# Kernel optimization log

Hardware: AMD Instinct MI355X
Metric: run time of the kernel (lower is better)

The kernel has to match this reference:

```python
import jax, jax.numpy as jnp
import numpy as np

DIM = 2048
NUM_HEADS = 16
HEAD_DIM = DIM // NUM_HEADS  # 128
LC = HEAD_DIM // 2           # 64 complex pairs per head
B, S = 2, 2048
EPS = 1e-6


def setup_inputs() -> dict:
    key = jax.random.key(0)
    ks = jax.random.split(key, 12)
    x = jax.random.normal(ks[0], (B, S, DIM), dtype=jnp.float32)
    # freqs: unit-modulus complex rotations stored as (cos, sin), shape [S,1,LC,2]
    theta = jax.random.uniform(ks[1], (S, 1, LC), dtype=jnp.float32) * (2.0 * np.pi)
    freqs = jnp.stack([jnp.cos(theta), jnp.sin(theta)], axis=-1)
    scale = 0.02
    wq = jax.random.normal(ks[2], (DIM, DIM), dtype=jnp.float32) * scale
    bq = jnp.zeros((DIM,), dtype=jnp.float32)
    wk = jax.random.normal(ks[3], (DIM, DIM), dtype=jnp.float32) * scale
    bk = jnp.zeros((DIM,), dtype=jnp.float32)
    wv = jax.random.normal(ks[4], (DIM, DIM), dtype=jnp.float32) * scale
    bv = jnp.zeros((DIM,), dtype=jnp.float32)
    wo = jax.random.normal(ks[5], (DIM, DIM), dtype=jnp.float32) * scale
    bo = jnp.zeros((DIM,), dtype=jnp.float32)
    gq = jnp.ones((DIM,), dtype=jnp.float32)   # RMSNorm weight for q
    gk = jnp.ones((DIM,), dtype=jnp.float32)   # RMSNorm weight for k
    return {"x": x, "freqs": freqs, "wq": wq, "bq": bq, "wk": wk, "bk": bk,
            "wv": wv, "bv": bv, "wo": wo, "bo": bo, "gq": gq, "gk": gk}


def _rms_norm(x, g):
    xf = x.astype(jnp.float32)
    y = xf * jax.lax.rsqrt(jnp.mean(xf * xf, axis=-1, keepdims=True) + EPS)
    return y.astype(x.dtype) * g


def _rope_apply(x, freqs):
    # x: [B,S,D] -> complex pairs [B,S,H,LC,2]; freqs: [S,1,LC,2] (cos,sin)
    b, s, _ = x.shape
    xp = x.astype(jnp.float32).reshape(b, s, NUM_HEADS, LC, 2)
    xr, xi = xp[..., 0], xp[..., 1]
    cr = freqs[None, :, :, :, 0]  # [1,S,1,LC]
    ci = freqs[None, :, :, :, 1]
    out_r = xr * cr - xi * ci
    out_i = xr * ci + xi * cr
    out = jnp.stack([out_r, out_i], axis=-1).reshape(b, s, DIM)
    return out.astype(x.dtype)


def _attention(q, k, v):
    # q,k,v: [B,S,D] -> multihead SDPA -> [B,S,D]
    b, s, _ = q.shape
    qh = q.reshape(b, s, NUM_HEADS, HEAD_DIM).transpose(0, 2, 1, 3)
    kh = k.reshape(b, s, NUM_HEADS, HEAD_DIM).transpose(0, 2, 1, 3)
    vh = v.reshape(b, s, NUM_HEADS, HEAD_DIM).transpose(0, 2, 1, 3)
    scale = 1.0 / np.sqrt(HEAD_DIM).astype(np.float32)
    scores = jnp.einsum('bhqd,bhkd->bhqk', qh, kh) * scale
    probs = jax.nn.softmax(scores, axis=-1)
    out = jnp.einsum('bhqk,bhkd->bhqd', probs, vh)
    return out.transpose(0, 2, 1, 3).reshape(b, s, DIM)


def reference(x, freqs, wq, bq, wk, bk, wv, bv, wo, bo, gq, gk):
    q = _rms_norm(x @ wq.T + bq, gq)
    k = _rms_norm(x @ wk.T + bk, gk)
    v = x @ wv.T + bv
    q = _rope_apply(q, freqs)
    k = _rope_apply(k, freqs)
    attn = _attention(q, k, v)
    return attn @ wo.T + bo
```

## Files before the change

kernel.cpp:

```cpp
#include <hip/hip_runtime.h>
#include <cstdint>

typedef __bf16 bf16;
typedef __bf16 bf16x8 __attribute__((ext_vector_type(8)));
typedef __bf16 bf16x4 __attribute__((ext_vector_type(4)));
typedef float f32x4 __attribute__((ext_vector_type(4)));

#define DIMN 2048
#define SEQ  2048
#define NH   16
#define HD   128

__device__ __forceinline__ void gld_lds16(const bf16* g, bf16* l) {
    __builtin_amdgcn_global_load_lds(
        (const __attribute__((address_space(1))) void*)g,
        (__attribute__((address_space(3))) void*)l,
        16, 0, 0);
}

__global__ __launch_bounds__(256) void cast_all(
    const float* __restrict__ x,
    const float* __restrict__ wq, const float* __restrict__ wk,
    const float* __restrict__ wv, const float* __restrict__ wo,
    bf16* __restrict__ xb,
    bf16* __restrict__ wqb, bf16* __restrict__ wkb,
    bf16* __restrict__ wvb, bf16* __restrict__ wob)
{
    int id = blockIdx.x;
    const float* src; bf16* dst; int i;
    if (id < 8192) { src = x; dst = xb; i = id * 256 + threadIdx.x; }
    else {
        id -= 8192;
        int w = id >> 12; id &= 4095;
        src = (w == 0) ? wq : (w == 1) ? wk : (w == 2) ? wv : wo;
        dst = (w == 0) ? wqb : (w == 1) ? wkb : (w == 2) ? wvb : wob;
        i = id * 256 + threadIdx.x;
    }
    float4 v = ((const float4*)src)[i];
    bf16x4 o;
    o[0] = (bf16)v.x; o[1] = (bf16)v.y; o[2] = (bf16)v.z; o[3] = (bf16)v.w;
    ((bf16x4*)dst)[i] = o;
}

template<int OUT_F32>
__global__ __launch_bounds__(256) void gemm_bt(
    const bf16* __restrict__ A,
    const bf16* __restrict__ Bw0, const bf16* __restrict__ Bw1, const bf16* __restrict__ Bw2,
    const float* __restrict__ bias0, const float* __restrict__ bias1, const float* __restrict__ bias2,
    void* __restrict__ C0, void* __restrict__ C1, void* __restrict__ C2)
{
    const int K = DIMN, N = DIMN;
    const bf16* Bw = Bw0; const float* bias = bias0; void* Cout = C0;
    if (blockIdx.z == 1) { Bw = Bw1; bias = bias1; Cout = C1; }
    if (blockIdx.z == 2) { Bw = Bw2; bias = bias2; Cout = C2; }

    __shared__ __attribute__((aligned(16))) bf16 As[128 * 64];
    __shared__ __attribute__((aligned(16))) bf16 Bs[128 * 64];

    const int t    = threadIdx.x;
    const int lane = t & 63, wave = t >> 6;
    const int l15  = lane & 15, quad = lane >> 4;
    const int wm   = (wave >> 1) * 64, wn = (wave & 1) * 64;
    const long bm  = (long)blockIdx.y * 128;
    const long bn  = (long)blockIdx.x * 128;

    const bf16* agp[4]; const bf16* bgp[4]; bf16* asd[4]; bf16* bsd[4];
#pragma unroll
    for (int it = 0; it < 4; it++) {
        int fs  = it * 256 + t;
        int row = fs >> 3;
        int gs  = (fs & 7) ^ (row & 7);
        agp[it] = A  + (bm + row) * (long)K + gs * 8;
        bgp[it] = Bw + (bn + row) * (long)K + gs * 8;
        asd[it] = As + fs * 8;
        bsd[it] = Bs + fs * 8;
    }
    const int swl = l15 & 7;

    f32x4 acc[4][4] = {};

    for (int k0 = 0; k0 < K; k0 += 64) {
#pragma unroll
        for (int it = 0; it < 4; it++) {
            gld_lds16(agp[it] + k0, asd[it]);
            gld_lds16(bgp[it] + k0, bsd[it]);
        }
        __syncthreads();

#pragma unroll
        for (int ks2 = 0; ks2 < 2; ks2++) {
            const int sw = ((ks2 * 4 + quad) ^ swl) * 8;
            bf16x8 af[4], bfr[4];
#pragma unroll
            for (int i = 0; i < 4; i++)
                af[i] = *(const bf16x8*)(As + (wm + i * 16 + l15) * 64 + sw);
#pragma unroll
            for (int j = 0; j < 4; j++)
                bfr[j] = *(const bf16x8*)(Bs + (wn + j * 16 + l15) * 64 + sw);
#pragma unroll
            for (int i = 0; i < 4; i++)
#pragma unroll
                for (int j = 0; j < 4; j++)
                    acc[i][j] = __builtin_amdgcn_mfma_f32_16x16x32_bf16(af[i], bfr[j], acc[i][j], 0, 0, 0);
        }
        __syncthreads();
    }

#pragma unroll
    for (int j = 0; j < 4; j++) {
        const long col = bn + wn + j * 16 + l15;
        const float bv = bias[col];
#pragma unroll
        for (int i = 0; i < 4; i++) {
            const long row0 = bm + wm + i * 16 + quad * 4;
#pragma unroll
            for (int r = 0; r < 4; r++) {
                float v = acc[i][j][r] + bv;
                if (OUT_F32) ((float*)Cout)[(row0 + r) * N + col] = v;
                else         ((bf16*)Cout)[(row0 + r) * N + col] = (bf16)v;
            }
        }
    }
}

__global__ __launch_bounds__(256) void norm_prep(
    bf16* __restrict__ q, bf16* __restrict__ k,
    const float* __restrict__ gq, const float* __restrict__ gk,
    const float* __restrict__ freqs,
    const bf16* __restrict__ vin, bf16* __restrict__ vt)
{
    const int id = blockIdx.x;
    const int t = threadIdx.x;
    if (id < 8192) {
        const int qk  = id >> 12;
        const int row = id & 4095;
        bf16* ptr = qk ? k : q;
        const float* g = qk ? gk : gq;
        const float osc = qk ? 1.0f : 0.08838834764831845f;
        const int s = row & (SEQ - 1);
        const int lane = t & 63, wave = t >> 6;

        bf16* base = ptr + (long)row * DIMN + t * 8;
        bf16x8 raw = *(const bf16x8*)base;
        float v[8]; float ss = 0.f;
#pragma unroll
        for (int j = 0; j < 8; j++) { v[j] = (float)raw[j]; ss += v[j] * v[j]; }
#pragma unroll
        for (int off = 32; off; off >>= 1) ss += __shfl_xor(ss, off, 64);
        __shared__ float red[4];
        if (lane == 0) red[wave] = ss;
        __syncthreads();
        float tot = red[0] + red[1] + red[2] + red[3];
        float rn = rsqrtf(tot * (1.0f / DIMN) + 1e-6f);

        const int e0 = t * 8;
        bf16x8 o;
#pragma unroll
        for (int pp = 0; pp < 4; pp++) {
            int e = e0 + pp * 2;
            float xr = v[pp * 2]     * rn * g[e];
            float xi = v[pp * 2 + 1] * rn * g[e + 1];
            int lc = (e >> 1) & 63;
            float cr = freqs[s * 128 + lc * 2];
            float ci = freqs[s * 128 + lc * 2 + 1];
            o[pp * 2]     = (bf16)((xr * cr - xi * ci) * osc);
            o[pp * 2 + 1] = (bf16)((xr * ci + xi * cr) * osc);
        }
        *(bf16x8*)base = o;
    } else {
        const int tid = id - 8192;
        const int b = tid >> 10, rem = tid & 1023;
        const int st = rem & 31, ct = rem >> 5;
        __shared__ float tile[64][65];
        const int tx = t & 63, ty = t >> 6;
#pragma unroll
        for (int ii = 0; ii < 16; ii++) {
            int r = ii * 4 + ty;
            tile[r][tx] = (float)vin[((long)(b * SEQ + st * 64 + r)) * DIMN + ct * 64 + tx];
        }
        __syncthreads();
#pragma unroll
        for (int ii = 0; ii < 16; ii++) {
            int c = ii * 4 + ty;
            vt[((long)(b * DIMN + ct * 64 + c)) * SEQ + st * 64 + tx] = (bf16)tile[tx][c];
        }
    }
}

__global__ __launch_bounds__(512, 2) void attention(
    const bf16* __restrict__ Q, const bf16* __restrict__ Kb,
    const bf16* __restrict__ Vt, bf16* __restrict__ O)
{
    __shared__ __attribute__((aligned(16))) bf16 Ksh[2][64 * 128];
    __shared__ __attribute__((aligned(16))) bf16 Vsh[2][128 * 64];
    __shared__ __attribute__((aligned(16))) bf16 Psh[8][32 * 72];
    __shared__ float Lsh[8][32];

    const int t = threadIdx.x;
    const int lane = t & 63, w = t >> 6;
    const int l15 = lane & 15, quad = lane >> 4;
    const int bh = blockIdx.x, b = bh >> 4, h = bh & 15;
    const int qt = blockIdx.y;
    const long qrow0 = (long)b * SEQ + qt * 256 + w * 32;
    const bf16* qbase = Q  + qrow0 * DIMN + h * HD;
    const bf16* kbase = Kb + (long)b * SEQ * DIMN + h * HD;
    const bf16* vbase = Vt + (long)bh * HD * SEQ;

    bf16x8 qf[2][4];
#pragma unroll
    for (int im = 0; im < 2; im++)
#pragma unroll
        for (int kd = 0; kd < 4; kd++)
            qf[im][kd] = *(const bf16x8*)(qbase + (long)(im * 16 + l15) * DIMN + kd * 32 + quad * 8);

    long koff[2], voff[2];
#pragma unroll
    for (int it = 0; it < 2; it++) {
        int fs = it * 512 + t;
        int kr = fs >> 4, kp = fs & 15;
        koff[it] = (long)kr * DIMN + (kp ^ (kr & 15)) * 8;
        int dr = fs >> 3, vp = fs & 7;
        voff[it] = (long)dr * SEQ + (vp ^ (dr & 7)) * 8;
    }

    f32x4 o_acc[2][8] = {};
    float Lt[2] = {0.f, 0.f};

#pragma unroll
    for (int it = 0; it < 2; it++) {
        gld_lds16(kbase + koff[it], &Ksh[0][(it * 512 + t) * 8]);
        gld_lds16(vbase + voff[it], &Vsh[0][(it * 512 + t) * 8]);
    }
    __syncthreads();

    for (int kt = 0; kt < 32; kt++) {
        const int cur = kt & 1;
        if (kt < 31) {
            const bf16* kg = kbase + (long)((kt + 1) * 64) * DIMN;
            const bf16* vg = vbase + (kt + 1) * 64;
#pragma unroll
            for (int it = 0; it < 2; it++) {
                gld_lds16(kg + koff[it], &Ksh[cur ^ 1][(it * 512 + t) * 8]);
                gld_lds16(vg + voff[it], &Vsh[cur ^ 1][(it * 512 + t) * 8]);
            }
        }
        const bf16* K0 = Ksh[cur];
        const bf16* V0 = Vsh[cur];

        f32x4 st[4][2] = {};
#pragma unroll
        for (int jk = 0; jk < 4; jk++)
#pragma unroll
            for (int kd = 0; kd < 4; kd++) {
                bf16x8 kf = *(const bf16x8*)(K0 + (jk * 16 + l15) * 128 + (((kd * 4 + quad) ^ l15) & 15) * 8);
                st[jk][0] = __builtin_amdgcn_mfma_f32_16x16x32_bf16(kf, qf[0][kd], st[jk][0], 0, 0, 0);
                st[jk][1] = __builtin_amdgcn_mfma_f32_16x16x32_bf16(kf, qf[1][kd], st[jk][1], 0, 0, 0);
            }

#pragma unroll
        for (int im = 0; im < 2; im++) {
            float part = 0.f;
#pragma unroll
            for (int jk = 0; jk < 4; jk++) {
                bf16x4 pk;
#pragma unroll
                for (int r = 0; r < 4; r++) {
                    float e = __expf(st[jk][im][r]);
                    part += e;
                    pk[r] = (bf16)e;
                }
                *(bf16x4*)(Psh[w] + (im * 16 + l15) * 72 + jk * 16 + quad * 4) = pk;
            }
            Lt[im] += part;
        }

#pragma unroll
        for (int kd2 = 0; kd2 < 2; kd2++) {
            bf16x8 pa[2];
            pa[0] = *(const bf16x8*)(Psh[w] + (l15)      * 72 + kd2 * 32 + quad * 8);
            pa[1] = *(const bf16x8*)(Psh[w] + (16 + l15) * 72 + kd2 * 32 + quad * 8);
#pragma unroll
            for (int dj = 0; dj < 8; dj++) {
                bf16x8 vfr = *(const bf16x8*)(V0 + (dj * 16 + l15) * 64 + (((kd2 * 4 + quad) ^ l15) & 7) * 8);
                o_acc[0][dj] = __builtin_amdgcn_mfma_f32_16x16x32_bf16(pa[0], vfr, o_acc[0][dj], 0, 0, 0);
                o_acc[1][dj] = __builtin_amdgcn_mfma_f32_16x16x32_bf16(pa[1], vfr, o_acc[1][dj], 0, 0, 0);
            }
        }
        __syncthreads();
    }

#pragma unroll
    for (int im = 0; im < 2; im++) {
        Lt[im] += __shfl_xor(Lt[im], 16, 64);
        Lt[im] += __shfl_xor(Lt[im], 32, 64);
    }
    if (quad == 0) { Lsh[w][l15] = Lt[0]; Lsh[w][16 + l15] = Lt[1]; }
    __syncthreads();

#pragma unroll
    for (int im = 0; im < 2; im++)
#pragma unroll
        for (int r = 0; r < 4; r++) {
            float inv = 1.0f / Lsh[w][im * 16 + quad * 4 + r];
            long orow = qrow0 + im * 16 + quad * 4 + r;
#pragma unroll
            for (int dj = 0; dj < 8; dj++)
                O[orow * DIMN + h * HD + dj * 16 + l15] = (bf16)(o_acc[im][dj][r] * inv);
        }
}

extern "C" void kernel_launch(void* const* d_in, const int* in_sizes, int n_in,
                              void* d_out, int out_size, void* d_ws, size_t ws_size,
                              hipStream_t stream) {
    const float* x     = (const float*)d_in[0];
    const float* freqs = (const float*)d_in[1];
    const float* wq    = (const float*)d_in[2];
    const float* bq    = (const float*)d_in[3];
    const float* wk    = (const float*)d_in[4];
    const float* bk    = (const float*)d_in[5];
    const float* wv    = (const float*)d_in[6];
    const float* bv    = (const float*)d_in[7];
    const float* wo    = (const float*)d_in[8];
    const float* bo    = (const float*)d_in[9];
    const float* gq    = (const float*)d_in[10];
    const float* gk    = (const float*)d_in[11];
    float* out = (float*)d_out;

    const size_t MAT  = (size_t)4096 * 2048 * 2;
    const size_t WMAT = (size_t)2048 * 2048 * 2;
    char* p = (char*)d_ws;
    bf16* xb  = (bf16*)p; p += MAT;
    bf16* wqb = (bf16*)p; p += WMAT;
    bf16* wkb = (bf16*)p; p += WMAT;
    bf16* wvb = (bf16*)p; p += WMAT;
    bf16* wob = (bf16*)p; p += WMAT;
    bf16* qb  = (bf16*)p; p += MAT;
    bf16* kb  = (bf16*)p; p += MAT;
    bf16* vb  = (bf16*)p; p += MAT;
    bf16* vt  = (bf16*)p; p += MAT;
    bf16* attn = qb;

    cast_all<<<24576, 256, 0, stream>>>(x, wq, wk, wv, wo, xb, wqb, wkb, wvb, wob);

    gemm_bt<0><<<dim3(16, 32, 3), 256, 0, stream>>>(xb, wqb, wkb, wvb,
                                                    bq, bk, bv, qb, kb, vb);
    norm_prep<<<10240, 256, 0, stream>>>(qb, kb, gq, gk, freqs, vb, vt);
    attention<<<dim3(32, 8), 512, 0, stream>>>(qb, kb, vt, attn);
    gemm_bt<1><<<dim3(16, 32, 1), 256, 0, stream>>>(attn, wob, wob, wob,
                                                    bo, bo, bo, out, out, out);
}
```

Measured before the change: 401.5 us.

## Replace QKV projection GEMM with 256x256-tile, 8-wave pipelined kernel

Adds a new gemm256 kernel for the fused QKV projection. It uses 256x256 output tiles with 512 threads and double-buffered LDS filled by direct global-to-LDS loads into XOR-swizzled rows. Compute is split into interleaved phases that issue the next tile's loads between MFMA groups, using vmcnt waits, barriers and setprio, and block IDs are remapped for L2 locality. The goal is more operand reuse per tile and better overlap of memory and compute than the old 256-thread kernel, at the cost of heavy register pressure and a fragile hand-made wait schedule.

```diff
diff --git a/kernel.cpp b/kernel.cpp
--- a/kernel.cpp
+++ b/kernel.cpp
@@ -123,6 +123,128 @@
     }
 }
 
+#define VMCNT3 asm volatile("s_waitcnt vmcnt(3)" ::: "memory")
+
+#define STAGE_AQ(bsel, kt, q) do {                                          \
+    const int row_ = (q) * 32 + arow_base;                                  \
+    gld_lds16(Ag + (long)row_ * DIMN + (kt) * 64 + ((ssg ^ (row_ & 7)) << 3), \
+              &As[bsel][(row_ * 8 + ssg) * 8]);                             \
+} while (0)
+
+#define STAGE_BU(bsel, kt, u) do {                                          \
+    const int row_ = (u) * 64 + srl;                                        \
+    gld_lds16(Bg + (long)row_ * DIMN + (kt) * 64 + ((ssg ^ (row_ & 7)) << 3), \
+              &Bs[bsel][(row_ * 8 + ssg) * 8]);                             \
+} while (0)
+
+#define PHASE(bsel, p0, STAGES, ...) do {                                   \
+    bf16x8 af_[2][2];                                                       \
+    _Pragma("unroll")                                                       \
+    for (int im = 0; im < 2; ++im) {                                        \
+        const int ar = wm * 128 + ((p0) * 2 + im) * 16 + l15;               \
+        _Pragma("unroll")                                                   \
+        for (int ks = 0; ks < 2; ++ks)                                      \
+            af_[im][ks] = *(const bf16x8*)(&As[bsel][(ar * 8 + ((ks * 4 + quad) ^ swl)) * 8]); \
+    }                                                                       \
+    if ((p0) == 0) {                                                        \
+        _Pragma("unroll")                                                   \
+        for (int j = 0; j < 4; ++j) {                                       \
+            const int br = wn * 64 + j * 16 + l15;                          \
+            _Pragma("unroll")                                               \
+            for (int ks = 0; ks < 2; ++ks)                                  \
+                bfrag[j][ks] = *(const bf16x8*)(&Bs[bsel][(br * 8 + ((ks * 4 + quad) ^ swl)) * 8]); \
+        }                                                                   \
+    }                                                                       \
+    STAGES;                                                                 \
+    asm volatile("" ::: "memory");                                          \
+    __builtin_amdgcn_s_barrier();                                           \
+    asm volatile("" ::: "memory");                                          \
+    __builtin_amdgcn_s_setprio(1);                                          \
+    _Pragma("unroll")                                                       \
+    for (int im = 0; im < 2; ++im)                                          \
+        _Pragma("unroll")                                                   \
+        for (int j = 0; j < 4; ++j)                                         \
+            _Pragma("unroll")                                               \
+            for (int ks = 0; ks < 2; ++ks)                                  \
+                acc[(p0) * 2 + im][j] = __builtin_amdgcn_mfma_f32_16x16x32_bf16( \
+                    af_[im][ks], bfrag[j][ks], acc[(p0) * 2 + im][j], 0, 0, 0); \
+    __builtin_amdgcn_s_setprio(0);                                          \
+    __VA_ARGS__;                                                            \
+    asm volatile("" ::: "memory");                                          \
+    __builtin_amdgcn_s_barrier();                                           \
+    asm volatile("" ::: "memory");                                          \
+} while (0)
+
+__global__ __launch_bounds__(512, 2) void gemm256(
+    const bf16* __restrict__ A,
+    const bf16* __restrict__ Bw0, const bf16* __restrict__ Bw1, const bf16* __restrict__ Bw2,
+    const float* __restrict__ bias0, const float* __restrict__ bias1, const float* __restrict__ bias2,
+    bf16* __restrict__ C0, bf16* __restrict__ C1, bf16* __restrict__ C2)
+{
+    const int N = DIMN;
+    const bf16* Bw = Bw0; const float* bias = bias0; bf16* Cout = C0;
+    if (blockIdx.z == 1) { Bw = Bw1; bias = bias1; Cout = C1; }
+    if (blockIdx.z == 2) { Bw = Bw2; bias = bias2; Cout = C2; }
+
+    __shared__ __attribute__((aligned(16))) bf16 As[2][256 * 64];
+    __shared__ __attribute__((aligned(16))) bf16 Bs[2][256 * 64];
+
+    const int t    = threadIdx.x;
+    const int lane = t & 63, wave = t >> 6;
+    const int l15  = lane & 15, quad = lane >> 4;
+    const int wm   = wave >> 2, wn = wave & 3;
+    const int swl  = l15 & 7;
+
+    const int id  = blockIdx.y * 8 + blockIdx.x;
+    const int wg  = (id & 7) * 16 + (id >> 3);
+    const long bm = (long)(wg >> 3) * 256;
+    const long bn = (long)(wg & 7) * 256;
+
+    const bf16* Ag = A  + bm * DIMN;
+    const bf16* Bg = Bw + bn * DIMN;
+
+    const int srl = t >> 3, ssg = t & 7;
+    const int arow_base = (srl & 31) + ((srl >> 5) << 7);
+
+    f32x4  acc[8][4] = {};
+    bf16x8 bfrag[4][2];
+
+    STAGE_BU(0, 0, 0); STAGE_BU(0, 0, 1); STAGE_BU(0, 0, 2); STAGE_BU(0, 0, 3);
+    STAGE_AQ(0, 0, 0); STAGE_AQ(0, 0, 1); STAGE_AQ(0, 0, 2); STAGE_AQ(0, 0, 3);
+    STAGE_AQ(1, 1, 0); STAGE_AQ(1, 1, 1); STAGE_AQ(1, 1, 2);
+    VMCNT3;
+    asm volatile("" ::: "memory");
+    __builtin_amdgcn_s_barrier();
+    asm volatile("" ::: "memory");
+
+    for (int it = 0; it < 16; ++it) {
+        const int tO  = 2 * it + 1;
+        const int tE2 = (2 * it + 2) & 31;
+        const int tO2 = (2 * it + 3) & 31;
+        PHASE(0, 0, { STAGE_BU(1, tO, 0); STAGE_BU(1, tO, 1); });
+        PHASE(0, 1, { STAGE_BU(1, tO, 2); STAGE_BU(1, tO, 3); });
+        PHASE(0, 2, { STAGE_AQ(1, tO, 3); STAGE_AQ(0, tE2, 0); });
+        PHASE(0, 3, { STAGE_AQ(0, tE2, 1); STAGE_AQ(0, tE2, 2); }, VMCNT3);
+        PHASE(1, 0, { STAGE_BU(0, tE2, 0); STAGE_BU(0, tE2, 1); });
+        PHASE(1, 1, { STAGE_BU(0, tE2, 2); STAGE_BU(0, tE2, 3); });
+        PHASE(1, 2, { STAGE_AQ(0, tE2, 3); STAGE_AQ(1, tO2, 0); });
+        PHASE(1, 3, { STAGE_AQ(1, tO2, 1); STAGE_AQ(1, tO2, 2); }, VMCNT3);
+    }
+
+#pragma unroll
+    for (int j = 0; j < 4; ++j) {
+        const long col = bn + wn * 64 + j * 16 + l15;
+        const float bv = bias[col];
+#pragma unroll
+        for (int i = 0; i < 8; ++i) {
+            const long row0 = bm + wm * 128 + i * 16 + quad * 4;
+#pragma unroll
+            for (int r = 0; r < 4; ++r)
+                Cout[(row0 + r) * N + col] = (bf16)(acc[i][j][r] + bv);
+        }
+    }
+}
+
 __global__ __launch_bounds__(256) void norm_prep(
     bf16* __restrict__ q, bf16* __restrict__ k,
     const float* __restrict__ gq, const float* __restrict__ gk,
@@ -342,8 +464,8 @@
 
     cast_all<<<24576, 256, 0, stream>>>(x, wq, wk, wv, wo, xb, wqb, wkb, wvb, wob);
 
-    gemm_bt<0><<<dim3(16, 32, 3), 256, 0, stream>>>(xb, wqb, wkb, wvb,
-                                                    bq, bk, bv, qb, kb, vb);
+    gemm256<<<dim3(8, 16, 3), 512, 0, stream>>>(xb, wqb, wkb, wvb,
+                                                bq, bk, bv, qb, kb, vb);
     norm_prep<<<10240, 256, 0, stream>>>(qb, kb, gq, gk, freqs, vb, vt);
     attention<<<dim3(32, 8), 512, 0, stream>>>(qb, kb, vt, attn);
     gemm_bt<1><<<dim3(16, 32, 1), 256, 0, stream>>>(attn, wob, wob, wob,
```

New measurement: 418.0 us. 1.04x slower.

## Compute V transposed directly in projection GEMM, use exp2 softmax, add setprio

Applied to the files above, without the earlier changes.

The V projection now swaps its operands (W_v as A, x as B), so the GEMM produces V^T and its epilogue writes straight into the transposed layout with a per-row bias. This drops the separate transpose pass in norm_prep and one intermediate buffer. Q is pre-scaled by log2(e)/sqrt(d) so the softmax can use exp2f instead of __expf. s_setprio is raised around the MFMA sections of attention. The transposed epilogue issues scattered 2-byte stores along the sequence dimension, which may coalesce poorly.

```diff
diff --git a/kernel.cpp b/kernel.cpp
--- a/kernel.cpp
+++ b/kernel.cpp
@@ -50,9 +50,11 @@
     void* __restrict__ C0, void* __restrict__ C1, void* __restrict__ C2)
 {
     const int K = DIMN, N = DIMN;
-    const bf16* Bw = Bw0; const float* bias = bias0; void* Cout = C0;
-    if (blockIdx.z == 1) { Bw = Bw1; bias = bias1; Cout = C1; }
-    if (blockIdx.z == 2) { Bw = Bw2; bias = bias2; Cout = C2; }
+    const int vtm = (!OUT_F32) && (blockIdx.z == 2);
+    const bf16* Ap; const bf16* Bp; const float* bias; void* Cout;
+    if (blockIdx.z == 0)      { Ap = A;   Bp = Bw0; bias = bias0; Cout = C0; }
+    else if (blockIdx.z == 1) { Ap = A;   Bp = Bw1; bias = bias1; Cout = C1; }
+    else                      { Ap = Bw2; Bp = A;   bias = bias2; Cout = C2; }
 
     __shared__ __attribute__((aligned(16))) bf16 As[128 * 64];
     __shared__ __attribute__((aligned(16))) bf16 Bs[128 * 64];
@@ -61,8 +63,8 @@
     const int lane = t & 63, wave = t >> 6;
     const int l15  = lane & 15, quad = lane >> 4;
     const int wm   = (wave >> 1) * 64, wn = (wave & 1) * 64;
-    const long bm  = (long)blockIdx.y * 128;
-    const long bn  = (long)blockIdx.x * 128;
+    const long bm = vtm ? (long)blockIdx.x * 128 : (long)blockIdx.y * 128;
+    const long bn = vtm ? (long)blockIdx.y * 128 : (long)blockIdx.x * 128;
 
     const bf16* agp[4]; const bf16* bgp[4]; bf16* asd[4]; bf16* bsd[4];
 #pragma unroll
@@ -70,8 +72,8 @@
         int fs  = it * 256 + t;
         int row = fs >> 3;
         int gs  = (fs & 7) ^ (row & 7);
-        agp[it] = A  + (bm + row) * (long)K + gs * 8;
-        bgp[it] = Bw + (bn + row) * (long)K + gs * 8;
+        agp[it] = Ap + (bm + row) * (long)K + gs * 8;
+        bgp[it] = Bp + (bn + row) * (long)K + gs * 8;
         asd[it] = As + fs * 8;
         bsd[it] = Bs + fs * 8;
     }
@@ -106,18 +108,34 @@
         __syncthreads();
     }
 
-#pragma unroll
-    for (int j = 0; j < 4; j++) {
-        const long col = bn + wn + j * 16 + l15;
-        const float bv = bias[col];
-#pragma unroll
-        for (int i = 0; i < 4; i++) {
-            const long row0 = bm + wm + i * 16 + quad * 4;
-#pragma unroll
-            for (int r = 0; r < 4; r++) {
-                float v = acc[i][j][r] + bv;
-                if (OUT_F32) ((float*)Cout)[(row0 + r) * N + col] = v;
-                else         ((bf16*)Cout)[(row0 + r) * N + col] = (bf16)v;
+    if (vtm) {
+#pragma unroll
+        for (int j = 0; j < 4; j++) {
+            const long col = bn + wn + j * 16 + l15;
+            const long cb = col >> 11, cs = col & (SEQ - 1);
+#pragma unroll
+            for (int i = 0; i < 4; i++) {
+                const long m0 = bm + wm + i * 16 + quad * 4;
+#pragma unroll
+                for (int r = 0; r < 4; r++)
+                    ((bf16*)Cout)[((cb * DIMN + m0 + r) * SEQ) + cs] =
+                        (bf16)(acc[i][j][r] + bias[m0 + r]);
+            }
+        }
+    } else {
+#pragma unroll
+        for (int j = 0; j < 4; j++) {
+            const long col = bn + wn + j * 16 + l15;
+            const float bv = bias[col];
+#pragma unroll
+            for (int i = 0; i < 4; i++) {
+                const long row0 = bm + wm + i * 16 + quad * 4;
+#pragma unroll
+                for (int r = 0; r < 4; r++) {
+                    float v = acc[i][j][r] + bv;
+                    if (OUT_F32) ((float*)Cout)[(row0 + r) * N + col] = v;
+                    else         ((bf16*)Cout)[(row0 + r) * N + col] = (bf16)v;
+                }
             }
         }
     }
@@ -126,65 +144,45 @@
 __global__ __launch_bounds__(256) void norm_prep(
     bf16* __restrict__ q, bf16* __restrict__ k,
     const float* __restrict__ gq, const float* __restrict__ gk,
-    const float* __restrict__ freqs,
-    const bf16* __restrict__ vin, bf16* __restrict__ vt)
+    const float* __restrict__ freqs)
 {
     const int id = blockIdx.x;
     const int t = threadIdx.x;
-    if (id < 8192) {
-        const int qk  = id >> 12;
-        const int row = id & 4095;
-        bf16* ptr = qk ? k : q;
-        const float* g = qk ? gk : gq;
-        const float osc = qk ? 1.0f : 0.08838834764831845f;
-        const int s = row & (SEQ - 1);
-        const int lane = t & 63, wave = t >> 6;
-
-        bf16* base = ptr + (long)row * DIMN + t * 8;
-        bf16x8 raw = *(const bf16x8*)base;
-        float v[8]; float ss = 0.f;
-#pragma unroll
-        for (int j = 0; j < 8; j++) { v[j] = (float)raw[j]; ss += v[j] * v[j]; }
-#pragma unroll
-        for (int off = 32; off; off >>= 1) ss += __shfl_xor(ss, off, 64);
-        __shared__ float red[4];
-        if (lane == 0) red[wave] = ss;
-        __syncthreads();
-        float tot = red[0] + red[1] + red[2] + red[3];
-        float rn = rsqrtf(tot * (1.0f / DIMN) + 1e-6f);
-
-        const int e0 = t * 8;
-        bf16x8 o;
-#pragma unroll
-        for (int pp = 0; pp < 4; pp++) {
-            int e = e0 + pp * 2;
-            float xr = v[pp * 2]     * rn * g[e];
-            float xi = v[pp * 2 + 1] * rn * g[e + 1];
-            int lc = (e >> 1) & 63;
-            float cr = freqs[s * 128 + lc * 2];
-            float ci = freqs[s * 128 + lc * 2 + 1];
-            o[pp * 2]     = (bf16)((xr * cr - xi * ci) * osc);
-            o[pp * 2 + 1] = (bf16)((xr * ci + xi * cr) * osc);
-        }
-        *(bf16x8*)base = o;
-    } else {
-        const int tid = id - 8192;
-        const int b = tid >> 10, rem = tid & 1023;
-        const int st = rem & 31, ct = rem >> 5;
-        __shared__ float tile[64][65];
-        const int tx = t & 63, ty = t >> 6;
-#pragma unroll
-        for (int ii = 0; ii < 16; ii++) {
-            int r = ii * 4 + ty;
-            tile[r][tx] = (float)vin[((long)(b * SEQ + st * 64 + r)) * DIMN + ct * 64 + tx];
-        }
-        __syncthreads();
-#pragma unroll
-        for (int ii = 0; ii < 16; ii++) {
-            int c = ii * 4 + ty;
-            vt[((long)(b * DIMN + ct * 64 + c)) * SEQ + st * 64 + tx] = (bf16)tile[tx][c];
-        }
-    }
+    const int qk  = id >> 12;
+    const int row = id & 4095;
+    bf16* ptr = qk ? k : q;
+    const float* g = qk ? gk : gq;
+    const float osc = qk ? 1.0f : 0.12753138080219222f;
+    const int s = row & (SEQ - 1);
+    const int lane = t & 63, wave = t >> 6;
+
+    bf16* base = ptr + (long)row * DIMN + t * 8;
+    bf16x8 raw = *(const bf16x8*)base;
+    float v[8]; float ss = 0.f;
+#pragma unroll
+    for (int j = 0; j < 8; j++) { v[j] = (float)raw[j]; ss += v[j] * v[j]; }
+#pragma unroll
+    for (int off = 32; off; off >>= 1) ss += __shfl_xor(ss, off, 64);
+    __shared__ float red[4];
+    if (lane == 0) red[wave] = ss;
+    __syncthreads();
+    float tot = red[0] + red[1] + red[2] + red[3];
+    float rn = rsqrtf(tot * (1.0f / DIMN) + 1e-6f);
+
+    const int e0 = t * 8;
+    bf16x8 o;
+#pragma unroll
+    for (int pp = 0; pp < 4; pp++) {
+        int e = e0 + pp * 2;
+        float xr = v[pp * 2]     * rn * g[e];
+        float xi = v[pp * 2 + 1] * rn * g[e + 1];
+        int lc = (e >> 1) & 63;
+        float cr = freqs[s * 128 + lc * 2];
+        float ci = freqs[s * 128 + lc * 2 + 1];
+        o[pp * 2]     = (bf16)((xr * cr - xi * ci) * osc);
+        o[pp * 2 + 1] = (bf16)((xr * ci + xi * cr) * osc);
+    }
+    *(bf16x8*)base = o;
 }
 
 __global__ __launch_bounds__(512, 2) void attention(
@@ -248,6 +246,7 @@
         const bf16* V0 = Vsh[cur];
 
         f32x4 st[4][2] = {};
+        __builtin_amdgcn_s_setprio(1);
 #pragma unroll
         for (int jk = 0; jk < 4; jk++)
 #pragma unroll
@@ -256,6 +255,7 @@
                 st[jk][0] = __builtin_amdgcn_mfma_f32_16x16x32_bf16(kf, qf[0][kd], st[jk][0], 0, 0, 0);
                 st[jk][1] = __builtin_amdgcn_mfma_f32_16x16x32_bf16(kf, qf[1][kd], st[jk][1], 0, 0, 0);
             }
+        __builtin_amdgcn_s_setprio(0);
 
 #pragma unroll
         for (int im = 0; im < 2; im++) {
@@ -265,7 +265,7 @@
                 bf16x4 pk;
 #pragma unroll
                 for (int r = 0; r < 4; r++) {
-                    float e = __expf(st[jk][im][r]);
+                    float e = exp2f(st[jk][im][r]);
                     part += e;
                     pk[r] = (bf16)e;
                 }
@@ -274,6 +274,7 @@
             Lt[im] += part;
         }
 
+        __builtin_amdgcn_s_setprio(1);
 #pragma unroll
         for (int kd2 = 0; kd2 < 2; kd2++) {
             bf16x8 pa[2];
@@ -286,6 +287,7 @@
                 o_acc[1][dj] = __builtin_amdgcn_mfma_f32_16x16x32_bf16(pa[1], vfr, o_acc[1][dj], 0, 0, 0);
             }
         }
+        __builtin_amdgcn_s_setprio(0);
         __syncthreads();
     }
 
@@ -336,15 +338,15 @@
     bf16* wob = (bf16*)p; p += WMAT;
     bf16* qb  = (bf16*)p; p += MAT;
     bf16* kb  = (bf16*)p; p += MAT;
-    bf16* vb  = (bf16*)p; p += MAT;
     bf16* vt  = (bf16*)p; p += MAT;
     bf16* attn = qb;
 
     cast_all<<<24576, 256, 0, stream>>>(x, wq, wk, wv, wo, xb, wqb, wkb, wvb, wob);
 
     gemm_bt<0><<<dim3(16, 32, 3), 256, 0, stream>>>(xb, wqb, wkb, wvb,
-                                                    bq, bk, bv, qb, kb, vb);
-    norm_prep<<<10240, 256, 0, stream>>>(qb, kb, gq, gk, freqs, vb, vt);
+                                                    bq, bk, bv, qb, kb, vt);
+
+    norm_prep<<<8192, 256, 0, stream>>>(qb, kb, gq, gk, freqs);
     attention<<<dim3(32, 8), 512, 0, stream>>>(qb, kb, vt, attn);
     gemm_bt<1><<<dim3(16, 32, 1), 256, 0, stream>>>(attn, wob, wob, wob,
                                                     bo, bo, bo, out, out, out);
```

Result: no change. 401.9 us (+0.1%).
